# Performance work log

Hardware: AMD Instinct MI355X
Metric: run time of the kernel (lower is better)

The kernel has to match this reference:

```python
import jax, jax.numpy as jnp
import numpy as np

IL = 9          # input_length
TL = 29         # total_length
P = TL - IL     # pred_length = 20
H = 512
W = 512


def _gather(imgs, yi, xi):
    # imgs: [B,1,H,W], yi/xi: [B,H,W] int32 -> [B,1,H,W]
    return jax.vmap(lambda im, y, x: im[0][y, x])(imgs, yi, xi)[:, None]


def _bilinear(imgs, cy, cx):
    # border padding, align_corners=True: coords already clipped to [0,dim-1]
    x0 = jnp.floor(cx)
    y0 = jnp.floor(cy)
    wx = (cx - x0)[:, None]  # [B,1,H,W]
    wy = (cy - y0)[:, None]
    x0i = jnp.clip(x0.astype(jnp.int32), 0, W - 1)
    y0i = jnp.clip(y0.astype(jnp.int32), 0, H - 1)
    x1i = jnp.clip(x0i + 1, 0, W - 1)
    y1i = jnp.clip(y0i + 1, 0, H - 1)
    v00 = _gather(imgs, y0i, x0i)
    v01 = _gather(imgs, y0i, x1i)
    v10 = _gather(imgs, y1i, x0i)
    v11 = _gather(imgs, y1i, x1i)
    return (1 - wy) * ((1 - wx) * v00 + wx * v01) + wy * ((1 - wx) * v10 + wx * v11)


def _nearest(imgs, cy, cx):
    # torch grid_sample 'nearest' uses round-half-to-even, same as jnp.round
    yi = jnp.clip(jnp.round(cy).astype(jnp.int32), 0, H - 1)
    xi = jnp.clip(jnp.round(cx).astype(jnp.int32), 0, W - 1)
    return _gather(imgs, yi, xi)


def setup_inputs() -> dict:
    key = jax.random.key(0)
    k1, k2, k3 = jax.random.split(key, 3)
    all_frames = jax.random.uniform(k1, (8, TL, H, W, 1), dtype=jnp.float32)
    motion = jax.random.normal(k2, (8, P * 2, H, W), dtype=jnp.float32)
    intensity = jax.random.normal(k3, (8, P, H, W), dtype=jnp.float32)
    return {"all_frames": all_frames, "motion": motion, "intensity": intensity}


def reference(all_frames, motion, intensity):
    all_frames = all_frames[:, :, :, :, :1]
    B = all_frames.shape[0]
    # last observed frame: [B,1,H,W]
    last = all_frames[:, IL - 1:IL, :, :, 0]
    motion_ = motion.reshape(B, P, 2, H, W)
    intensity_ = intensity.reshape(B, P, 1, H, W)

    gy, gx = jnp.meshgrid(jnp.arange(H, dtype=jnp.float32),
                          jnp.arange(W, dtype=jnp.float32), indexing="ij")

    def step(carry, xs):
        flow, inten = xs  # [B,2,H,W], [B,1,H,W]
        cx = jnp.clip(gx + flow[:, 0], 0.0, W - 1)
        cy = jnp.clip(gy + flow[:, 1], 0.0, H - 1)
        bili = _bilinear(carry, cy, cx)
        nxt = _nearest(carry, cy, cx) + inten
        return nxt, (nxt, bili)

    xs = (jnp.swapaxes(motion_, 0, 1), jnp.swapaxes(intensity_, 0, 1))
    _, (series, bilis) = jax.lax.scan(step, last, xs)
    # series/bilis: [P,B,1,H,W] -> [B,P,H,W]
    evo_result = jnp.swapaxes(series, 0, 1).reshape(B, P, H, W) / 128.0
    evo_motion = jnp.swapaxes(bilis, 0, 1).reshape(B, P, H, W)
    return evo_result, evo_motion, motion_
```

## Files before the change

### kernel.cpp

```cpp
#include <hip/hip_runtime.h>

#define W_  512
#define H_  512
#define HW  (512 * 512)
#define P_  20
#define B_  8
#define TL_ 29
#define IL_ 9

#define NB   1024
#define NT   256
#define BPB  (NB / B_)
#define TPB  (BPB * NT)
#define PPT  (HW / TPB)

#define WS_MISMATCH 0
#define WS_GCNT     32
#define WS_GGO      64
#define WS_SCNT     96
#define WS_SGO      128
#define WS_FBAR(b)  (160 + 32 * (b))
#define WS_FGO(b)   (448 + 32 * (b))

__device__ __forceinline__ unsigned rel_faa(unsigned* p, unsigned v) {
    return __hip_atomic_fetch_add(p, v, __ATOMIC_RELAXED, __HIP_MEMORY_SCOPE_AGENT);
}
__device__ __forceinline__ void rel_st(unsigned* p, unsigned v) {
    __hip_atomic_store(p, v, __ATOMIC_RELAXED, __HIP_MEMORY_SCOPE_AGENT);
}
__device__ __forceinline__ unsigned rel_ld(unsigned* p) {
    return __hip_atomic_load(p, __ATOMIC_RELAXED, __HIP_MEMORY_SCOPE_AGENT);
}
__device__ __forceinline__ float mall_ldf(const float* p) {
    return __hip_atomic_load(p, __ATOMIC_RELAXED, __HIP_MEMORY_SCOPE_AGENT);
}
__device__ __forceinline__ void mall_stf(float* p, float v) {
    __hip_atomic_store(p, v, __ATOMIC_RELAXED, __HIP_MEMORY_SCOPE_AGENT);
}

__global__ __launch_bounds__(NT, 4) void fused_scan(
    const float* __restrict__ frames,
    const float* __restrict__ motion,
    const float* __restrict__ intensity,
    float*                    evo_result,
    float* __restrict__       evo_motion,
    float* __restrict__       motion_out,
    unsigned*                 ws)
{
    const int bid = blockIdx.x;
    const int b   = bid & 7;
    const int inb = ((bid >> 3) << 8) + threadIdx.x;

    __shared__ unsigned s_flag;
    if (threadIdx.x == 0) {
        unsigned xcc;
        asm volatile("s_getreg_b32 %0, hwreg(HW_REG_XCC_ID)" : "=s"(xcc));
        if ((int)(xcc & 7) != b) rel_st(ws + WS_MISMATCH, 1u);
        asm volatile("s_waitcnt vmcnt(0)" ::: "memory");
    }
    __syncthreads();
    if (threadIdx.x == 0) {
        unsigned old = rel_faa(ws + WS_GCNT, 1u);
        if (old + 1 == NB) rel_st(ws + WS_GGO, 1u);
        else while (rel_ld(ws + WS_GGO) < 1u) __builtin_amdgcn_s_sleep(2);
        s_flag = rel_ld(ws + WS_MISMATCH);
        asm volatile("" ::: "memory");
    }
    __syncthreads();
    const bool fast = (s_flag == 0);

    const float* frame0 = frames + ((long)b * TL_ + (IL_ - 1)) * HW;

    for (int p = 0; p < P_; ++p) {
        const float scale = (p == 0) ? 1.0f : 128.0f;
        const float* prev = (p == 0) ? frame0
                                     : evo_result + ((long)b * P_ + (p - 1)) * HW;
        const long moP = ((long)b * (2 * P_) + 2 * p) * HW;
        const long ioP = ((long)b * P_ + p) * HW;

        for (int j = 0; j < PPT; ++j) {
            const int rem = j * TPB + inb;
            const int y   = rem >> 9;
            const int x   = rem & (W_ - 1);
            const long mo0 = moP + rem;
            const long io  = ioP + rem;

            const float f0 = __builtin_nontemporal_load(motion + mo0);
            const float f1 = __builtin_nontemporal_load(motion + mo0 + HW);
            const float iv = __builtin_nontemporal_load(intensity + io);
            __builtin_nontemporal_store(f0, motion_out + mo0);
            __builtin_nontemporal_store(f1, motion_out + mo0 + HW);

            const float cx = fminf(fmaxf((float)x + f0, 0.0f), 511.0f);
            const float cy = fminf(fmaxf((float)y + f1, 0.0f), 511.0f);
            const float x0f = floorf(cx), y0f = floorf(cy);
            const float wx = cx - x0f, wy = cy - y0f;
            const int x0 = (int)x0f, y0 = (int)y0f;
            const int x1 = min(x0 + 1, W_ - 1), y1 = min(y0 + 1, H_ - 1);
            const int xi = (int)rintf(cx);
            const int yi = (int)rintf(cy);

            float v00, v01, v10, v11, vn;
            if (p == 0) {
                v00 = prev[y0 * W_ + x0];  v01 = prev[y0 * W_ + x1];
                v10 = prev[y1 * W_ + x0];  v11 = prev[y1 * W_ + x1];
                vn  = prev[yi * W_ + xi];
            } else if (fast) {
                v00 = prev[y0 * W_ + x0];  v01 = prev[y0 * W_ + x1];
                v10 = prev[y1 * W_ + x0];  v11 = prev[y1 * W_ + x1];
                vn  = prev[yi * W_ + xi];
            } else {
                v00 = mall_ldf(prev + y0 * W_ + x0);
                v01 = mall_ldf(prev + y0 * W_ + x1);
                v10 = mall_ldf(prev + y1 * W_ + x0);
                v11 = mall_ldf(prev + y1 * W_ + x1);
                vn  = mall_ldf(prev + yi * W_ + xi);
            }

            const float bil = scale * ((1.0f - wy) * ((1.0f - wx) * v00 + wx * v01)
                                             + wy  * ((1.0f - wx) * v10 + wx * v11));
            const float res = (scale * vn + iv) * 0.0078125f;

            if (fast) evo_result[io] = res;
            else      mall_stf(evo_result + io, res);
            __builtin_nontemporal_store(bil, evo_motion + io);
        }

        if (p != P_ - 1) {
            __syncthreads();
            if (threadIdx.x == 0) {
                const unsigned gen = (unsigned)(p + 1);
                if (fast) {
                    unsigned old = rel_faa(ws + WS_FBAR(b), 1u);
                    if (old + 1 == gen * BPB) rel_st(ws + WS_FGO(b), gen);
                    else while (rel_ld(ws + WS_FGO(b)) < gen)
                        __builtin_amdgcn_s_sleep(2);
                } else {
                    unsigned old = rel_faa(ws + WS_SCNT, 1u);
                    if (old + 1 == gen * NB) rel_st(ws + WS_SGO, gen);
                    else while (rel_ld(ws + WS_SGO) < gen)
                        __builtin_amdgcn_s_sleep(2);
                }
                asm volatile("" ::: "memory");
            }
            __syncthreads();
        }
    }
}

extern "C" void kernel_launch(void* const* d_in, const int* in_sizes, int n_in,
                              void* d_out, int out_size, void* d_ws, size_t ws_size,
                              hipStream_t stream)
{
    const float* frames    = (const float*)d_in[0];
    const float* motion    = (const float*)d_in[1];
    const float* intensity = (const float*)d_in[2];

    float* out        = (float*)d_out;
    float* evo_result = out;
    float* evo_motion = out + (long)B_ * P_ * HW;
    float* motion_out = out + 2L * B_ * P_ * HW;
    unsigned* ws      = (unsigned*)d_ws;

    hipMemsetAsync(ws, 0, 4096, stream);

    fused_scan<<<dim3(NB), dim3(NT), 0, stream>>>(
        frames, motion, intensity, evo_result, evo_motion, motion_out, ws);
}
```

Measured before the change: 376.4 us.

## Prefetch next step's motion and intensity into registers before the grid barrier

Loads the motion and intensity values for step p+1 into per-thread register arrays before waiting at the inter-step barrier, so their global-memory latency overlaps the barrier wait. The point loops are fully unrolled over PPT elements. This raises register pressure (three PPT-sized arrays plus indices), which may reduce occupancy under the 4-waves launch bound.

```diff
diff --git a/kernel.cpp b/kernel.cpp
--- a/kernel.cpp
+++ b/kernel.cpp
@@ -70,29 +70,46 @@
     const bool fast = (s_flag == 0);
 
     const float* frame0 = frames + ((long)b * TL_ + (IL_ - 1)) * HW;
+    const long   ioB    = (long)b * P_ * HW;
+    const long   moB    = (long)b * (2 * P_) * HW;
+
+    int rem[PPT];
+    #pragma unroll
+    for (int j = 0; j < PPT; ++j) rem[j] = j * TPB + inb;
+
+    float f0v[PPT], f1v[PPT], ivv[PPT];
+    {
+        const long moP = moB;
+        const long ioP = ioB;
+        #pragma unroll
+        for (int j = 0; j < PPT; ++j) {
+            f0v[j] = __builtin_nontemporal_load(motion + moP + rem[j]);
+            f1v[j] = __builtin_nontemporal_load(motion + moP + HW + rem[j]);
+            ivv[j] = __builtin_nontemporal_load(intensity + ioP + rem[j]);
+        }
+    }
 
     for (int p = 0; p < P_; ++p) {
         const float scale = (p == 0) ? 1.0f : 128.0f;
         const float* prev = (p == 0) ? frame0
-                                     : evo_result + ((long)b * P_ + (p - 1)) * HW;
-        const long moP = ((long)b * (2 * P_) + 2 * p) * HW;
-        const long ioP = ((long)b * P_ + p) * HW;
+                                     : evo_result + ioB + (long)(p - 1) * HW;
+        const long moP = moB + (long)(2 * p) * HW;
+        const long ioP = ioB + (long)p * HW;
 
+        #pragma unroll
         for (int j = 0; j < PPT; ++j) {
-            const int rem = j * TPB + inb;
-            const int y   = rem >> 9;
-            const int x   = rem & (W_ - 1);
-            const long mo0 = moP + rem;
-            const long io  = ioP + rem;
+            __builtin_nontemporal_store(f0v[j], motion_out + moP + rem[j]);
+            __builtin_nontemporal_store(f1v[j], motion_out + moP + HW + rem[j]);
+        }
 
-            const float f0 = __builtin_nontemporal_load(motion + mo0);
-            const float f1 = __builtin_nontemporal_load(motion + mo0 + HW);
-            const float iv = __builtin_nontemporal_load(intensity + io);
-            __builtin_nontemporal_store(f0, motion_out + mo0);
-            __builtin_nontemporal_store(f1, motion_out + mo0 + HW);
+        #pragma unroll
+        for (int j = 0; j < PPT; ++j) {
+            const int r = rem[j];
+            const int y = r >> 9;
+            const int x = r & (W_ - 1);
 
-            const float cx = fminf(fmaxf((float)x + f0, 0.0f), 511.0f);
-            const float cy = fminf(fmaxf((float)y + f1, 0.0f), 511.0f);
+            const float cx = fminf(fmaxf((float)x + f0v[j], 0.0f), 511.0f);
+            const float cy = fminf(fmaxf((float)y + f1v[j], 0.0f), 511.0f);
             const float x0f = floorf(cx), y0f = floorf(cy);
             const float wx = cx - x0f, wy = cy - y0f;
             const int x0 = (int)x0f, y0 = (int)y0f;
@@ -101,11 +118,7 @@
             const int yi = (int)rintf(cy);
 
             float v00, v01, v10, v11, vn;
-            if (p == 0) {
-                v00 = prev[y0 * W_ + x0];  v01 = prev[y0 * W_ + x1];
-                v10 = prev[y1 * W_ + x0];  v11 = prev[y1 * W_ + x1];
-                vn  = prev[yi * W_ + xi];
-            } else if (fast) {
+            if (fast || p == 0) {
                 v00 = prev[y0 * W_ + x0];  v01 = prev[y0 * W_ + x1];
                 v10 = prev[y1 * W_ + x0];  v11 = prev[y1 * W_ + x1];
                 vn  = prev[yi * W_ + xi];
@@ -119,14 +132,23 @@
 
             const float bil = scale * ((1.0f - wy) * ((1.0f - wx) * v00 + wx * v01)
                                              + wy  * ((1.0f - wx) * v10 + wx * v11));
-            const float res = (scale * vn + iv) * 0.0078125f;
+            const float res = (scale * vn + ivv[j]) * 0.0078125f;
 
-            if (fast) evo_result[io] = res;
-            else      mall_stf(evo_result + io, res);
-            __builtin_nontemporal_store(bil, evo_motion + io);
+            if (fast) evo_result[ioP + r] = res;
+            else      mall_stf(evo_result + ioP + r, res);
+            __builtin_nontemporal_store(bil, evo_motion + ioP + r);
         }
 
         if (p != P_ - 1) {
+            const long moN = moP + 2 * HW;
+            const long ioN = ioP + HW;
+            #pragma unroll
+            for (int j = 0; j < PPT; ++j) {
+                f0v[j] = __builtin_nontemporal_load(motion + moN + rem[j]);
+                f1v[j] = __builtin_nontemporal_load(motion + moN + HW + rem[j]);
+                ivv[j] = __builtin_nontemporal_load(intensity + ioN + rem[j]);
+            }
+
             __syncthreads();
             if (threadIdx.x == 0) {
                 const unsigned gen = (unsigned)(p + 1);
```

Measured after the change: 349.0 us. 7.3% less time.
